# Optimization experiments

Hardware: AMD Instinct MI355X
Metric: run time of the kernel (lower is better)

## Reference

```python
import jax, jax.numpy as jnp
import numpy as np

D = 768; H = 12; L = 6; B = 8; S = 256; DH = D // H
_SCALE = 1.0 / float(np.sqrt(D))
_SCALE_FFN2 = 1.0 / float(np.sqrt(4 * D))


def _ln(x, g, b):
    m = jnp.mean(x, axis=-1, keepdims=True)
    v = jnp.mean((x - m) ** 2, axis=-1, keepdims=True)
    return (x - m) / jnp.sqrt(v + 1e-12) * g + b


def _mhsa(q_in, k_in, v_in, w, bias, mask, scale):
    # w: [3, D, D], bias: [3, D]; mask: [B, S_k]
    def proj(t, W, b):
        return (t @ W + b).reshape(t.shape[0], t.shape[1], H, DH).transpose(0, 2, 1, 3)
    q = proj(q_in, w[0], bias[0])
    k = proj(k_in, w[1], bias[1])
    v = proj(v_in, w[2], bias[2])
    s = jnp.einsum('bhqd,bhkd->bhqk', q, k) * scale
    s = s - 10000.0 * (1.0 - mask[:, None, None, :].astype(s.dtype))
    p = jax.nn.softmax(s, axis=-1)
    h = jnp.einsum('bhqk,bhkd->bhqd', p, v)
    return h.transpose(0, 2, 1, 3).reshape(q_in.shape[0], q_in.shape[1], D)


def _ffn(x, w1, b1, w2, b2):
    return jax.nn.gelu(x @ w1 + b1, approximate=False) @ w2 + b2


def setup_inputs() -> dict:
    key = jax.random.key(0)
    ks = jax.random.split(key, 16)
    inp = {
        'x': jax.random.normal(ks[0], (B, S, D), jnp.float32),
        'y': jax.random.normal(ks[1], (B, S, D), jnp.float32),
        'x_mask': jnp.ones((B, S), jnp.int32),
        'y_mask': jnp.ones((B, S), jnp.int32),
        'ax_w': jax.random.normal(ks[2], (L, 3, D, D), jnp.float32) * _SCALE,
        'ax_b': jnp.zeros((L, 3, D), jnp.float32),
        'cx_w': jax.random.normal(ks[3], (L, 3, D, D), jnp.float32) * _SCALE,
        'cx_b': jnp.zeros((L, 3, D), jnp.float32),
        'fx_w1': jax.random.normal(ks[4], (L, D, 4 * D), jnp.float32) * _SCALE,
        'fx_b1': jnp.zeros((L, 4 * D), jnp.float32),
        'fx_w2': jax.random.normal(ks[5], (L, 4 * D, D), jnp.float32) * _SCALE_FFN2,
        'fx_b2': jnp.zeros((L, D), jnp.float32),
        'ay_w': jax.random.normal(ks[6], (L, 3, D, D), jnp.float32) * _SCALE,
        'ay_b': jnp.zeros((L, 3, D), jnp.float32),
        'cy_w': jax.random.normal(ks[7], (L, 3, D, D), jnp.float32) * _SCALE,
        'cy_b': jnp.zeros((L, 3, D), jnp.float32),
        'fy_w1': jax.random.normal(ks[8], (L, D, 4 * D), jnp.float32) * _SCALE,
        'fy_b1': jnp.zeros((L, 4 * D), jnp.float32),
        'fy_w2': jax.random.normal(ks[9], (L, 4 * D, D), jnp.float32) * _SCALE_FFN2,
        'fy_b2': jnp.zeros((L, D), jnp.float32),
        'lnx_g': jnp.ones((3, D), jnp.float32),
        'lnx_b': jnp.zeros((3, D), jnp.float32),
        'lny_g': jnp.ones((3, D), jnp.float32),
        'lny_b': jnp.zeros((3, D), jnp.float32),
    }
    return inp


def reference(x, y, x_mask, y_mask, ax_w, ax_b, cx_w, cx_b, fx_w1, fx_b1, fx_w2, fx_b2,
              ay_w, ay_b, cy_w, cy_b, fy_w1, fy_b1, fy_w2, fy_b2,
              lnx_g, lnx_b, lny_g, lny_b):
    inv_sqrt_dh = 1.0 / float(np.sqrt(DH))
    params = dict(ax_w=ax_w, ax_b=ax_b, cx_w=cx_w, cx_b=cx_b,
                  fx_w1=fx_w1, fx_b1=fx_b1, fx_w2=fx_w2, fx_b2=fx_b2,
                  ay_w=ay_w, ay_b=ay_b, cy_w=cy_w, cy_b=cy_b,
                  fy_w1=fy_w1, fy_b1=fy_b1, fy_w2=fy_w2, fy_b2=fy_b2)

    def layer(carry, p):
        xc, yc = carry
        xc = _ln(xc + _mhsa(xc, xc, xc, p['ax_w'], p['ax_b'], x_mask, inv_sqrt_dh), lnx_g[0], lnx_b[0])
        yc = _ln(yc + _mhsa(yc, yc, yc, p['ay_w'], p['ay_b'], y_mask, inv_sqrt_dh), lny_g[0], lny_b[0])
        xc = _ln(xc + _mhsa(xc, yc, yc, p['cx_w'], p['cx_b'], y_mask, inv_sqrt_dh), lnx_g[1], lnx_b[1])
        yc = _ln(yc + _mhsa(yc, xc, xc, p['cy_w'], p['cy_b'], x_mask, inv_sqrt_dh), lny_g[1], lny_b[1])
        xc = _ln(xc + _ffn(xc, p['fx_w1'], p['fx_b1'], p['fx_w2'], p['fx_b2']), lnx_g[2], lnx_b[2])
        yc = _ln(yc + _ffn(yc, p['fy_w1'], p['fy_b1'], p['fy_w2'], p['fy_b2']), lny_g[2], lny_b[2])
        return (xc, yc), None

    (x, y), _ = jax.lax.scan(layer, (x, y), params)
    return jnp.stack([x, y])  # [2, B, S, D]
```

## Files before the change

kernel.cpp:

```cpp
#include <hip/hip_runtime.h>
#include <math.h>

constexpr int D = 768;
constexpr int H = 12;
constexpr int L = 6;
constexpr int B = 8;
constexpr int S = 256;
constexpr int DH = 64;
constexpr int M = B * S;
constexpr int D4 = 4 * D;

typedef _Float16 v2h __attribute__((ext_vector_type(2)));
typedef _Float16 v4h __attribute__((ext_vector_type(4)));
typedef _Float16 v8h __attribute__((ext_vector_type(8)));
typedef __fp16 f16x2 __attribute__((ext_vector_type(2)));
typedef float v4f __attribute__((ext_vector_type(4)));

__device__ inline void cvt_split(float x, float y, v2h& hi, v2h& lo) {
    f16x2 h = __builtin_amdgcn_cvt_pkrtz(x, y);
    float rx = x - (float)h[0];
    float ry = y - (float)h[1];
    f16x2 l = __builtin_amdgcn_cvt_pkrtz(rx, ry);
    hi = __builtin_bit_cast(v2h, h);
    lo = __builtin_bit_cast(v2h, l);
}

__global__ __launch_bounds__(256) void gemm_mfma(
    const float* __restrict__ Aq0, const float* __restrict__ Akv0,
    const float* __restrict__ W0,  const float* __restrict__ bias0, float* __restrict__ C0,
    const float* __restrict__ Aq1, const float* __restrict__ Akv1,
    const float* __restrict__ W1,  const float* __restrict__ bias1, float* __restrict__ C1,
    int qsplit, int Kstride, int kchunk, int N, int n_per_mat, int nblks, int act, int atomic)
{
    const int z = blockIdx.z;
    const float* __restrict__ Aq  = z ? Aq1  : Aq0;
    const float* __restrict__ Akv = z ? Akv1 : Akv0;
    const float* __restrict__ Wb  = z ? W1   : W0;
    const float* __restrict__ biasz = z ? bias1 : bias0;
    float* __restrict__ C = z ? C1 : C0;

    const int bx = blockIdx.x;
    const int nb = bx % nblks;
    const int kpart = bx / nblks;
    const int n0 = nb * 128;
    const int m0 = blockIdx.y * 128;
    const float* __restrict__ A = ((n0 < qsplit) ? Aq : Akv) + (size_t)kpart * kchunk;
    const int sub = n0 / n_per_mat;
    const int nc0 = n0 - sub * n_per_mat;
    const float* __restrict__ W = Wb + (size_t)sub * Kstride * n_per_mat
                                     + (size_t)kpart * kchunk * n_per_mat;
    const float* __restrict__ bias = (kpart == 0) ? biasz : nullptr;

    const int tid = threadIdx.x;
    const int lane = tid & 63;
    const int wave = tid >> 6;
    const int wm = (wave & 1) * 64;
    const int wn = (wave >> 1) * 64;

    __shared__ _Float16 sm[4 * 128 * 40];
    _Float16* Ah = sm;
    _Float16* Al = sm + 128 * 40;
    _Float16* Bh = sm + 2 * 128 * 40;
    _Float16* Bl = sm + 3 * 128 * 40;

    v4f acc[4][4];
    #pragma unroll
    for (int i = 0; i < 4; ++i)
        #pragma unroll
        for (int j = 0; j < 4; ++j)
            acc[i][j] = (v4f){0.f, 0.f, 0.f, 0.f};

    const int ar = tid >> 3;
    const int ac = (tid & 7) * 4;
    const int bn = tid & 127;
    const int bk0 = (tid >> 7) * 16;

    const int fm = lane & 15;
    const int fk = (lane >> 4) * 8;

    float4 av[4], av2[4];
    float bv[16], bv2[16];
    #pragma unroll
    for (int i = 0; i < 4; ++i)
        av[i] = *(const float4*)(A + (size_t)(m0 + ar + 32 * i) * Kstride + ac);
    #pragma unroll
    for (int j = 0; j < 16; ++j)
        bv[j] = W[(size_t)(bk0 + j) * n_per_mat + nc0 + bn];

    for (int k0 = 0; k0 < kchunk; k0 += 32) {
        __syncthreads();

        #pragma unroll
        for (int i = 0; i < 4; ++i) {
            v2h h0, l0, h1, l1;
            cvt_split(av[i].x, av[i].y, h0, l0);
            cvt_split(av[i].z, av[i].w, h1, l1);
            v4h hh, ll;
            hh[0] = h0[0]; hh[1] = h0[1]; hh[2] = h1[0]; hh[3] = h1[1];
            ll[0] = l0[0]; ll[1] = l0[1]; ll[2] = l1[0]; ll[3] = l1[1];
            *(v4h*)&Ah[(ar + 32 * i) * 40 + ac] = hh;
            *(v4h*)&Al[(ar + 32 * i) * 40 + ac] = ll;
        }
        {
            v8h bha, bhb, bla, blb;
            #pragma unroll
            for (int j = 0; j < 4; ++j) {
                v2h h, l;
                cvt_split(bv[2 * j], bv[2 * j + 1], h, l);
                bha[2 * j] = h[0]; bha[2 * j + 1] = h[1];
                bla[2 * j] = l[0]; bla[2 * j + 1] = l[1];
            }
            #pragma unroll
            for (int j = 0; j < 4; ++j) {
                v2h h, l;
                cvt_split(bv[8 + 2 * j], bv[8 + 2 * j + 1], h, l);
                bhb[2 * j] = h[0]; bhb[2 * j + 1] = h[1];
                blb[2 * j] = l[0]; blb[2 * j + 1] = l[1];
            }
            *(v8h*)&Bh[bn * 40 + bk0] = bha;
            *(v8h*)&Bh[bn * 40 + bk0 + 8] = bhb;
            *(v8h*)&Bl[bn * 40 + bk0] = bla;
            *(v8h*)&Bl[bn * 40 + bk0 + 8] = blb;
        }
        __syncthreads();

        if (k0 + 32 < kchunk) {
            #pragma unroll
            for (int i = 0; i < 4; ++i)
                av2[i] = *(const float4*)(A + (size_t)(m0 + ar + 32 * i) * Kstride + k0 + 32 + ac);
            #pragma unroll
            for (int j = 0; j < 16; ++j)
                bv2[j] = W[(size_t)(k0 + 32 + bk0 + j) * n_per_mat + nc0 + bn];
        }

        v8h fah[4], fal[4], fbh[4], fbl[4];
        #pragma unroll
        for (int i = 0; i < 4; ++i) {
            fah[i] = *(v8h*)&Ah[(wm + i * 16 + fm) * 40 + fk];
            fal[i] = *(v8h*)&Al[(wm + i * 16 + fm) * 40 + fk];
        }
        #pragma unroll
        for (int j = 0; j < 4; ++j) {
            fbh[j] = *(v8h*)&Bh[(wn + j * 16 + fm) * 40 + fk];
            fbl[j] = *(v8h*)&Bl[(wn + j * 16 + fm) * 40 + fk];
        }
        #pragma unroll
        for (int i = 0; i < 4; ++i)
            #pragma unroll
            for (int j = 0; j < 4; ++j) {
                acc[i][j] = __builtin_amdgcn_mfma_f32_16x16x32_f16(fah[i], fbh[j], acc[i][j], 0, 0, 0);
                acc[i][j] = __builtin_amdgcn_mfma_f32_16x16x32_f16(fah[i], fbl[j], acc[i][j], 0, 0, 0);
                acc[i][j] = __builtin_amdgcn_mfma_f32_16x16x32_f16(fal[i], fbh[j], acc[i][j], 0, 0, 0);
            }

        #pragma unroll
        for (int i = 0; i < 4; ++i) av[i] = av2[i];
        #pragma unroll
        for (int j = 0; j < 16; ++j) bv[j] = bv2[j];
    }

    const int er = (lane >> 4) * 4;
    const int ec = lane & 15;
    #pragma unroll
    for (int j = 0; j < 4; ++j) {
        const int col = n0 + wn + j * 16 + ec;
        const float bs = bias ? bias[col] : 0.0f;
        #pragma unroll
        for (int i = 0; i < 4; ++i) {
            #pragma unroll
            for (int r = 0; r < 4; ++r) {
                const int row = m0 + wm + i * 16 + er + r;
                float v = acc[i][j][r] + bs;
                if (act == 1)
                    v = 0.5f * v * (1.0f + erff(v * 0.7071067811865476f));
                if (atomic)
                    atomicAdd(&C[(size_t)row * N + col], v);
                else
                    C[(size_t)row * N + col] = v;
            }
        }
    }
}

__global__ __launch_bounds__(256) void attn_kernel(
    const float* __restrict__ qkv0, const int* __restrict__ mask0, float* __restrict__ hout0,
    const float* __restrict__ qkv1, const int* __restrict__ mask1, float* __restrict__ hout1)
{
    const float* __restrict__ qkv = blockIdx.z ? qkv1 : qkv0;
    const int* __restrict__ mask = blockIdx.z ? mask1 : mask0;
    float* __restrict__ hout = blockIdx.z ? hout1 : hout0;

    const int blk = blockIdx.x;
    const int qt = blk & 3;
    const int bh = blk >> 2;
    const int head = bh % H;
    const int b = bh / H;
    const int tid = threadIdx.x;
    const int wave = tid >> 6;
    const int lane = tid & 63;
    const int qloc = lane & 15;
    const int rg = lane >> 4;

    __shared__ _Float16 KVh[64 * 72];
    __shared__ _Float16 KVl[64 * 72];
    __shared__ _Float16 Ph[4][16 * 72];
    __shared__ _Float16 Pl[4][16 * 72];
    __shared__ float mpen[256];

    mpen[tid] = -10000.0f * (1.0f - (float)mask[b * S + tid]);

    const int qrow = b * S + qt * 64 + wave * 16 + qloc;
    const float* qptr = qkv + (size_t)qrow * 2304 + head * DH + rg * 8;
    v8h qh[2], ql[2];
    #pragma unroll
    for (int ks = 0; ks < 2; ++ks) {
        float4 a = *(const float4*)(qptr + ks * 32);
        float4 c = *(const float4*)(qptr + ks * 32 + 4);
        v2h h, l;
        v8h hh, ll;
        cvt_split(a.x, a.y, h, l); hh[0] = h[0]; hh[1] = h[1]; ll[0] = l[0]; ll[1] = l[1];
        cvt_split(a.z, a.w, h, l); hh[2] = h[0]; hh[3] = h[1]; ll[2] = l[0]; ll[3] = l[1];
        cvt_split(c.x, c.y, h, l); hh[4] = h[0]; hh[5] = h[1]; ll[4] = l[0]; ll[5] = l[1];
        cvt_split(c.z, c.w, h, l); hh[6] = h[0]; hh[7] = h[1]; ll[6] = l[0]; ll[7] = l[1];
        qh[ks] = hh; ql[ks] = ll;
    }

    v4f acc_s[16];
    #pragma unroll
    for (int i = 0; i < 16; ++i) acc_s[i] = (v4f){0.f, 0.f, 0.f, 0.f};

    const float* kbase = qkv + 768 + head * DH;
    const float* vbase = qkv + 1536 + head * DH;

    const int skey = tid & 63;
    const int sseg = (tid >> 6) * 16;
    #pragma unroll
    for (int t = 0; t < 4; ++t) {
        __syncthreads();
        {
            const float* src = kbase + (size_t)(b * S + t * 64 + skey) * 2304 + sseg;
            float4 a = ((const float4*)src)[0];
            float4 c = ((const float4*)src)[1];
            float4 e = ((const float4*)src)[2];
            float4 f = ((const float4*)src)[3];
            v2h h, l;
            v8h hA, lA, hB, lB;
            cvt_split(a.x, a.y, h, l); hA[0] = h[0]; hA[1] = h[1]; lA[0] = l[0]; lA[1] = l[1];
            cvt_split(a.z, a.w, h, l); hA[2] = h[0]; hA[3] = h[1]; lA[2] = l[0]; lA[3] = l[1];
            cvt_split(c.x, c.y, h, l); hA[4] = h[0]; hA[5] = h[1]; lA[4] = l[0]; lA[5] = l[1];
            cvt_split(c.z, c.w, h, l); hA[6] = h[0]; hA[7] = h[1]; lA[6] = l[0]; lA[7] = l[1];
            cvt_split(e.x, e.y, h, l); hB[0] = h[0]; hB[1] = h[1]; lB[0] = l[0]; lB[1] = l[1];
            cvt_split(e.z, e.w, h, l); hB[2] = h[0]; hB[3] = h[1]; lB[2] = l[0]; lB[3] = l[1];
            cvt_split(f.x, f.y, h, l); hB[4] = h[0]; hB[5] = h[1]; lB[4] = l[0]; lB[5] = l[1];
            cvt_split(f.z, f.w, h, l); hB[6] = h[0]; hB[7] = h[1]; lB[6] = l[0]; lB[7] = l[1];
            *(v8h*)&KVh[skey * 72 + sseg] = hA;
            *(v8h*)&KVh[skey * 72 + sseg + 8] = hB;
            *(v8h*)&KVl[skey * 72 + sseg] = lA;
            *(v8h*)&KVl[skey * 72 + sseg + 8] = lB;
        }
        __syncthreads();
        #pragma unroll
        for (int sub = 0; sub < 4; ++sub) {
            v8h kh[2], kl[2];
            #pragma unroll
            for (int ks = 0; ks < 2; ++ks) {
                kh[ks] = *(v8h*)&KVh[(sub * 16 + qloc) * 72 + ks * 32 + rg * 8];
                kl[ks] = *(v8h*)&KVl[(sub * 16 + qloc) * 72 + ks * 32 + rg * 8];
            }
            v4f acc = acc_s[t * 4 + sub];
            #pragma unroll
            for (int ks = 0; ks < 2; ++ks) {
                acc = __builtin_amdgcn_mfma_f32_16x16x32_f16(kh[ks], qh[ks], acc, 0, 0, 0);
                acc = __builtin_amdgcn_mfma_f32_16x16x32_f16(kh[ks], ql[ks], acc, 0, 0, 0);
                acc = __builtin_amdgcn_mfma_f32_16x16x32_f16(kl[ks], qh[ks], acc, 0, 0, 0);
            }
            acc_s[t * 4 + sub] = acc;
        }
    }

    float mx = -3.0e38f;
    #pragma unroll
    for (int mt = 0; mt < 16; ++mt) {
        float4 mp = *(const float4*)&mpen[mt * 16 + rg * 4];
        v4f s = acc_s[mt];
        s[0] = s[0] * 0.125f + mp.x;
        s[1] = s[1] * 0.125f + mp.y;
        s[2] = s[2] * 0.125f + mp.z;
        s[3] = s[3] * 0.125f + mp.w;
        acc_s[mt] = s;
        mx = fmaxf(mx, fmaxf(fmaxf(s[0], s[1]), fmaxf(s[2], s[3])));
    }
    mx = fmaxf(mx, __shfl_xor(mx, 16, 64));
    mx = fmaxf(mx, __shfl_xor(mx, 32, 64));
    float sum = 0.f;
    #pragma unroll
    for (int mt = 0; mt < 16; ++mt) {
        v4f s = acc_s[mt];
        s[0] = __expf(s[0] - mx);
        s[1] = __expf(s[1] - mx);
        s[2] = __expf(s[2] - mx);
        s[3] = __expf(s[3] - mx);
        acc_s[mt] = s;
        sum += (s[0] + s[1]) + (s[2] + s[3]);
    }
    sum += __shfl_xor(sum, 16, 64);
    sum += __shfl_xor(sum, 32, 64);
    const float inv = 1.0f / sum;

    v4f acc_o[4];
    #pragma unroll
    for (int j = 0; j < 4; ++j) acc_o[j] = (v4f){0.f, 0.f, 0.f, 0.f};

    const int vk4 = (tid & 15) * 4;
    const int vd4 = (tid >> 4) * 4;
    #pragma unroll
    for (int t = 0; t < 4; ++t) {
        __syncthreads();
        #pragma unroll
        for (int sub = 0; sub < 4; ++sub) {
            v4f p = acc_s[t * 4 + sub];
            v2h h01, l01, h23, l23;
            cvt_split(p[0], p[1], h01, l01);
            cvt_split(p[2], p[3], h23, l23);
            *(v2h*)&Ph[wave][qloc * 72 + sub * 16 + rg * 4] = h01;
            *(v2h*)&Ph[wave][qloc * 72 + sub * 16 + rg * 4 + 2] = h23;
            *(v2h*)&Pl[wave][qloc * 72 + sub * 16 + rg * 4] = l01;
            *(v2h*)&Pl[wave][qloc * 72 + sub * 16 + rg * 4 + 2] = l23;
        }
        {
            v4h rh[4], rl[4];
            #pragma unroll
            for (int i = 0; i < 4; ++i) {
                const float4 vv = *(const float4*)(vbase + (size_t)(b * S + t * 64 + vk4 + i) * 2304 + vd4);
                v2h h0, l0, h1, l1;
                cvt_split(vv.x, vv.y, h0, l0);
                cvt_split(vv.z, vv.w, h1, l1);
                rh[0][i] = h0[0]; rh[1][i] = h0[1]; rh[2][i] = h1[0]; rh[3][i] = h1[1];
                rl[0][i] = l0[0]; rl[1][i] = l0[1]; rl[2][i] = l1[0]; rl[3][i] = l1[1];
            }
            #pragma unroll
            for (int j = 0; j < 4; ++j) {
                *(v4h*)&KVh[(vd4 + j) * 72 + vk4] = rh[j];
                *(v4h*)&KVl[(vd4 + j) * 72 + vk4] = rl[j];
            }
        }
        __syncthreads();
        v8h pah[2], pal[2];
        #pragma unroll
        for (int ks = 0; ks < 2; ++ks) {
            pah[ks] = *(v8h*)&Ph[wave][qloc * 72 + ks * 32 + rg * 8];
            pal[ks] = *(v8h*)&Pl[wave][qloc * 72 + ks * 32 + rg * 8];
        }
        #pragma unroll
        for (int j = 0; j < 4; ++j) {
            v4f acc = acc_o[j];
            #pragma unroll
            for (int ks = 0; ks < 2; ++ks) {
                v8h vbh = *(v8h*)&KVh[(j * 16 + qloc) * 72 + ks * 32 + rg * 8];
                v8h vbl = *(v8h*)&KVl[(j * 16 + qloc) * 72 + ks * 32 + rg * 8];
                acc = __builtin_amdgcn_mfma_f32_16x16x32_f16(pah[ks], vbh, acc, 0, 0, 0);
                acc = __builtin_amdgcn_mfma_f32_16x16x32_f16(pah[ks], vbl, acc, 0, 0, 0);
                acc = __builtin_amdgcn_mfma_f32_16x16x32_f16(pal[ks], vbh, acc, 0, 0, 0);
            }
            acc_o[j] = acc;
        }
    }

    #pragma unroll
    for (int r = 0; r < 4; ++r) {
        const float invr = __shfl(inv, rg * 4 + r, 64);
        const size_t row = (size_t)(b * S + qt * 64 + wave * 16 + rg * 4 + r);
        #pragma unroll
        for (int j = 0; j < 4; ++j)
            hout[row * D + head * DH + j * 16 + qloc] = acc_o[j][r] * invr;
    }
}

__global__ __launch_bounds__(256) void ln_res_kernel(
    float* __restrict__ x0, const float* __restrict__ h0,
    const float* __restrict__ g0, const float* __restrict__ bb0,
    float* __restrict__ x1, const float* __restrict__ h1,
    const float* __restrict__ g1, const float* __restrict__ bb1)
{
    float* __restrict__ x = blockIdx.y ? x1 : x0;
    const float* __restrict__ h = blockIdx.y ? h1 : h0;
    const float* __restrict__ g = blockIdx.y ? g1 : g0;
    const float* __restrict__ bb = blockIdx.y ? bb1 : bb0;

    const int row = blockIdx.x;
    const int tid = threadIdx.x;
    const int wave = tid >> 6;
    const int lane = tid & 63;
    __shared__ float red[4];

    float v[3];
    #pragma unroll
    for (int i = 0; i < 3; ++i) {
        int c = tid + 256 * i;
        v[i] = x[(size_t)row * D + c] + h[(size_t)row * D + c];
    }
    float s = v[0] + v[1] + v[2];
    #pragma unroll
    for (int o = 32; o > 0; o >>= 1) s += __shfl_xor(s, o, 64);
    if (lane == 0) red[wave] = s;
    __syncthreads();
    const float mean = (red[0] + red[1] + red[2] + red[3]) * (1.0f / 768.0f);

    float qs = 0.f;
    #pragma unroll
    for (int i = 0; i < 3; ++i) { float d = v[i] - mean; qs += d * d; }
    #pragma unroll
    for (int o = 32; o > 0; o >>= 1) qs += __shfl_xor(qs, o, 64);
    __syncthreads();
    if (lane == 0) red[wave] = qs;
    __syncthreads();
    const float var = (red[0] + red[1] + red[2] + red[3]) * (1.0f / 768.0f);
    const float rstd = rsqrtf(var + 1e-12f);

    #pragma unroll
    for (int i = 0; i < 3; ++i) {
        int c = tid + 256 * i;
        x[(size_t)row * D + c] = (v[i] - mean) * rstd * g[c] + bb[c];
    }
}

extern "C" void kernel_launch(void* const* d_in, const int* in_sizes, int n_in,
                              void* d_out, int out_size, void* d_ws, size_t ws_size,
                              hipStream_t stream)
{
    const float* x    = (const float*)d_in[0];
    const float* y    = (const float*)d_in[1];
    const int*   xm   = (const int*)d_in[2];
    const int*   ym   = (const int*)d_in[3];
    const float* ax_w = (const float*)d_in[4];
    const float* ax_b = (const float*)d_in[5];
    const float* cx_w = (const float*)d_in[6];
    const float* cx_b = (const float*)d_in[7];
    const float* fx_w1 = (const float*)d_in[8];
    const float* fx_b1 = (const float*)d_in[9];
    const float* fx_w2 = (const float*)d_in[10];
    const float* fx_b2 = (const float*)d_in[11];
    const float* ay_w = (const float*)d_in[12];
    const float* ay_b = (const float*)d_in[13];
    const float* cy_w = (const float*)d_in[14];
    const float* cy_b = (const float*)d_in[15];
    const float* fy_w1 = (const float*)d_in[16];
    const float* fy_b1 = (const float*)d_in[17];
    const float* fy_w2 = (const float*)d_in[18];
    const float* fy_b2 = (const float*)d_in[19];
    const float* lnx_g = (const float*)d_in[20];
    const float* lnx_b = (const float*)d_in[21];
    const float* lny_g = (const float*)d_in[22];
    const float* lny_b = (const float*)d_in[23];

    float* xc = (float*)d_out;
    float* yc = xc + (size_t)M * D;

    const size_t need = ((size_t)2 * M * D4 + (size_t)2 * M * D) * sizeof(float);
    const bool big = ws_size >= need;
    float* ws0 = (float*)d_ws;
    float* qkvx = ws0;
    float* qkvy = big ? ws0 + (size_t)M * D4 : ws0;
    float* hbx = ws0 + (big ? (size_t)2 * M * D4 : (size_t)M * D4);
    float* hby = big ? hbx + (size_t)M * D : hbx;

    (void)hipMemcpyAsync(xc, x, (size_t)M * D * sizeof(float), hipMemcpyDeviceToDevice, stream);
    (void)hipMemcpyAsync(yc, y, (size_t)M * D * sizeof(float), hipMemcpyDeviceToDevice, stream);

    const dim3 blk(256);
    constexpr int KSPLIT = 4;

    auto qkv_gemm = [&](const float* aq0, const float* akv0, const float* w0, const float* bi0, float* c0,
                        const float* aq1, const float* akv1, const float* w1, const float* bi1, float* c1,
                        int nz) {
        gemm_mfma<<<dim3(2304 / 128, M / 128, nz), blk, 0, stream>>>(
            aq0, akv0, w0, bi0, c0, aq1, akv1, w1, bi1, c1,
            768, D, D, 2304, 768, 2304 / 128, 0, 0);
    };
    auto ffn1_gemm = [&](const float* a0, const float* w0, const float* bi0, float* c0,
                         const float* a1, const float* w1, const float* bi1, float* c1, int nz) {
        gemm_mfma<<<dim3(D4 / 128, M / 128, nz), blk, 0, stream>>>(
            a0, a0, w0, bi0, c0, a1, a1, w1, bi1, c1,
            0, D, D, D4, D4, D4 / 128, 1, 0);
    };
    auto ffn2_gemm_split = [&](const float* a0, const float* w0, const float* bi0, float* c0,
                               const float* a1, const float* w1, const float* bi1, float* c1, int nz) {
        gemm_mfma<<<dim3((D / 128) * KSPLIT, M / 128, nz), blk, 0, stream>>>(
            a0, a0, w0, bi0, c0, a1, a1, w1, bi1, c1,
            0, D4, D4 / KSPLIT, D, D, D / 128, 0, 1);
    };
    auto ffn2_gemm_seq = [&](const float* a0, const float* w0, const float* bi0, float* c0,
                             const float* a1, const float* w1, const float* bi1, float* c1, int nz) {
        gemm_mfma<<<dim3(D / 128, M / 128, nz), blk, 0, stream>>>(
            a0, a0, w0, bi0, c0, a1, a1, w1, bi1, c1,
            0, D4, D4, D, D, D / 128, 0, 0);
    };
    auto attn = [&](const float* q0, const int* m0_, float* h0,
                    const float* q1, const int* m1_, float* h1, int nz) {
        attn_kernel<<<dim3(B * H * 4, 1, nz), blk, 0, stream>>>(q0, m0_, h0, q1, m1_, h1);
    };
    auto ln = [&](float* x0, const float* h0, const float* g0, const float* b0,
                  float* x1, const float* h1, const float* g1, const float* b1, int ny) {
        ln_res_kernel<<<dim3(M, ny), blk, 0, stream>>>(x0, h0, g0, b0, x1, h1, g1, b1);
    };

    for (int l = 0; l < L; ++l) {
        const size_t wo = (size_t)l * 3 * D * D;
        const size_t bo = (size_t)l * 3 * D;
        const size_t f1o = (size_t)l * D * D4;
        const size_t f1bo = (size_t)l * D4;
        const size_t f2o = (size_t)l * D4 * D;
        const size_t f2bo = (size_t)l * D;

        if (big) {
            qkv_gemm(xc, xc, ax_w + wo, ax_b + bo, qkvx,
                     yc, yc, ay_w + wo, ay_b + bo, qkvy, 2);
            attn(qkvx, xm, hbx, qkvy, ym, hby, 2);
            ln(xc, hbx, lnx_g, lnx_b, yc, hby, lny_g, lny_b, 2);
            qkv_gemm(xc, yc, cx_w + wo, cx_b + bo, qkvx,
                     xc, yc, cx_w + wo, cx_b + bo, qkvx, 1);
            attn(qkvx, ym, hbx, qkvx, ym, hbx, 1);
            ln(xc, hbx, lnx_g + D, lnx_b + D, xc, hbx, lnx_g + D, lnx_b + D, 1);
            qkv_gemm(yc, xc, cy_w + wo, cy_b + bo, qkvy,
                     yc, xc, cy_w + wo, cy_b + bo, qkvy, 1);
            attn(qkvy, xm, hby, qkvy, xm, hby, 1);
            ln(yc, hby, lny_g + D, lny_b + D, yc, hby, lny_g + D, lny_b + D, 1);
            ffn1_gemm(xc, fx_w1 + f1o, fx_b1 + f1bo, qkvx,
                      yc, fy_w1 + f1o, fy_b1 + f1bo, qkvy, 2);
            (void)hipMemsetAsync(hbx, 0, (size_t)2 * M * D * sizeof(float), stream);
            ffn2_gemm_split(qkvx, fx_w2 + f2o, fx_b2 + f2bo, hbx,
                            qkvy, fy_w2 + f2o, fy_b2 + f2bo, hby, 2);
            ln(xc, hbx, lnx_g + 2 * D, lnx_b + 2 * D,
               yc, hby, lny_g + 2 * D, lny_b + 2 * D, 2);
        } else {
            qkv_gemm(xc, xc, ax_w + wo, ax_b + bo, qkvx, xc, xc, ax_w + wo, ax_b + bo, qkvx, 1);
            attn(qkvx, xm, hbx, qkvx, xm, hbx, 1);
            ln(xc, hbx, lnx_g, lnx_b, xc, hbx, lnx_g, lnx_b, 1);
            qkv_gemm(yc, yc, ay_w + wo, ay_b + bo, qkvy, yc, yc, ay_w + wo, ay_b + bo, qkvy, 1);
            attn(qkvy, ym, hby, qkvy, ym, hby, 1);
            ln(yc, hby, lny_g, lny_b, yc, hby, lny_g, lny_b, 1);
            qkv_gemm(xc, yc, cx_w + wo, cx_b + bo, qkvx, xc, yc, cx_w + wo, cx_b + bo, qkvx, 1);
            attn(qkvx, ym, hbx, qkvx, ym, hbx, 1);
            ln(xc, hbx, lnx_g + D, lnx_b + D, xc, hbx, lnx_g + D, lnx_b + D, 1);
            qkv_gemm(yc, xc, cy_w + wo, cy_b + bo, qkvy, yc, xc, cy_w + wo, cy_b + bo, qkvy, 1);
            attn(qkvy, xm, hby, qkvy, xm, hby, 1);
            ln(yc, hby, lny_g + D, lny_b + D, yc, hby, lny_g + D, lny_b + D, 1);
            ffn1_gemm(xc, fx_w1 + f1o, fx_b1 + f1bo, qkvx, xc, fx_w1 + f1o, fx_b1 + f1bo, qkvx, 1);
            ffn2_gemm_seq(qkvx, fx_w2 + f2o, fx_b2 + f2bo, hbx, qkvx, fx_w2 + f2o, fx_b2 + f2bo, hbx, 1);
            ln(xc, hbx, lnx_g + 2 * D, lnx_b + 2 * D, xc, hbx, lnx_g + 2 * D, lnx_b + 2 * D, 1);
            ffn1_gemm(yc, fy_w1 + f1o, fy_b1 + f1bo, qkvy, yc, fy_w1 + f1o, fy_b1 + f1bo, qkvy, 1);
            ffn2_gemm_seq(qkvy, fy_w2 + f2o, fy_b2 + f2bo, hby, qkvy, fy_w2 + f2o, fy_b2 + f2bo, hby, 1);
            ln(yc, hby, lny_g + 2 * D, lny_b + 2 * D, yc, hby, lny_g + 2 * D, lny_b + 2 * D, 1);
        }
    }
}
```

Baseline: 3.026 ms.

## Store activations as pre-split fp16 hi/lo pairs produced by producer epilogues

```diff
diff --git a/kernel.cpp b/kernel.cpp
--- a/kernel.cpp
+++ b/kernel.cpp
@@ -25,26 +25,39 @@
     lo = __builtin_bit_cast(v2h, l);
 }
 
+__device__ inline void split1(float v, _Float16& hi, _Float16& lo) {
+    f16x2 h = __builtin_amdgcn_cvt_pkrtz(v, v);
+    float r = v - (float)h[0];
+    f16x2 l = __builtin_amdgcn_cvt_pkrtz(r, r);
+    hi = (_Float16)h[0];
+    lo = (_Float16)l[0];
+}
+
 __global__ __launch_bounds__(256) void gemm_mfma(
-    const float* __restrict__ Aq0, const float* __restrict__ Akv0,
-    const float* __restrict__ W0,  const float* __restrict__ bias0, float* __restrict__ C0,
-    const float* __restrict__ Aq1, const float* __restrict__ Akv1,
-    const float* __restrict__ W1,  const float* __restrict__ bias1, float* __restrict__ C1,
-    int qsplit, int Kstride, int kchunk, int N, int n_per_mat, int nblks, int act, int atomic)
+    const _Float16* __restrict__ Aq0, const _Float16* __restrict__ Akv0,
+    const float* __restrict__ W0,  const float* __restrict__ bias0,
+    float* __restrict__ C0, _Float16* __restrict__ P0,
+    const _Float16* __restrict__ Aq1, const _Float16* __restrict__ Akv1,
+    const float* __restrict__ W1,  const float* __restrict__ bias1,
+    float* __restrict__ C1, _Float16* __restrict__ P1,
+    int qsplit, int Kstride, int kchunk, int N, int n_per_mat, int nblks,
+    int act, int atomic, int outp, long asize, long csize)
 {
     const int z = blockIdx.z;
-    const float* __restrict__ Aq  = z ? Aq1  : Aq0;
-    const float* __restrict__ Akv = z ? Akv1 : Akv0;
+    const _Float16* __restrict__ Aq  = z ? Aq1  : Aq0;
+    const _Float16* __restrict__ Akv = z ? Akv1 : Akv0;
     const float* __restrict__ Wb  = z ? W1   : W0;
     const float* __restrict__ biasz = z ? bias1 : bias0;
     float* __restrict__ C = z ? C1 : C0;
+    _Float16* __restrict__ Ph_g = z ? P1 : P0;
 
     const int bx = blockIdx.x;
     const int nb = bx % nblks;
     const int kpart = bx / nblks;
     const int n0 = nb * 128;
     const int m0 = blockIdx.y * 128;
-    const float* __restrict__ A = ((n0 < qsplit) ? Aq : Akv) + (size_t)kpart * kchunk;
+    const _Float16* __restrict__ Ah_g = ((n0 < qsplit) ? Aq : Akv) + (size_t)kpart * kchunk;
+    const _Float16* __restrict__ Al_g = Ah_g + asize;
     const int sub = n0 / n_per_mat;
     const int nc0 = n0 - sub * n_per_mat;
     const float* __restrict__ W = Wb + (size_t)sub * Kstride * n_per_mat
@@ -70,19 +83,21 @@
         for (int j = 0; j < 4; ++j)
             acc[i][j] = (v4f){0.f, 0.f, 0.f, 0.f};
 
-    const int ar = tid >> 3;
-    const int ac = (tid & 7) * 4;
+    const int ar = tid >> 2;
+    const int ac = (tid & 3) * 8;
     const int bn = tid & 127;
     const int bk0 = (tid >> 7) * 16;
 
     const int fm = lane & 15;
     const int fk = (lane >> 4) * 8;
 
-    float4 av[4], av2[4];
+    v8h avh[2], avl[2], avh2[2], avl2[2];
     float bv[16], bv2[16];
     #pragma unroll
-    for (int i = 0; i < 4; ++i)
-        av[i] = *(const float4*)(A + (size_t)(m0 + ar + 32 * i) * Kstride + ac);
+    for (int i = 0; i < 2; ++i) {
+        avh[i] = *(const v8h*)(Ah_g + (size_t)(m0 + ar + 64 * i) * Kstride + ac);
+        avl[i] = *(const v8h*)(Al_g + (size_t)(m0 + ar + 64 * i) * Kstride + ac);
+    }
     #pragma unroll
     for (int j = 0; j < 16; ++j)
         bv[j] = W[(size_t)(bk0 + j) * n_per_mat + nc0 + bn];
@@ -91,15 +106,9 @@
         __syncthreads();
 
         #pragma unroll
-        for (int i = 0; i < 4; ++i) {
-            v2h h0, l0, h1, l1;
-            cvt_split(av[i].x, av[i].y, h0, l0);
-            cvt_split(av[i].z, av[i].w, h1, l1);
-            v4h hh, ll;
-            hh[0] = h0[0]; hh[1] = h0[1]; hh[2] = h1[0]; hh[3] = h1[1];
-            ll[0] = l0[0]; ll[1] = l0[1]; ll[2] = l1[0]; ll[3] = l1[1];
-            *(v4h*)&Ah[(ar + 32 * i) * 40 + ac] = hh;
-            *(v4h*)&Al[(ar + 32 * i) * 40 + ac] = ll;
+        for (int i = 0; i < 2; ++i) {
+            *(v8h*)&Ah[(ar + 64 * i) * 40 + ac] = avh[i];
+            *(v8h*)&Al[(ar + 64 * i) * 40 + ac] = avl[i];
         }
         {
             v8h bha, bhb, bla, blb;
@@ -126,8 +135,10 @@
 
         if (k0 + 32 < kchunk) {
             #pragma unroll
-            for (int i = 0; i < 4; ++i)
-                av2[i] = *(const float4*)(A + (size_t)(m0 + ar + 32 * i) * Kstride + k0 + 32 + ac);
+            for (int i = 0; i < 2; ++i) {
+                avh2[i] = *(const v8h*)(Ah_g + (size_t)(m0 + ar + 64 * i) * Kstride + k0 + 32 + ac);
+                avl2[i] = *(const v8h*)(Al_g + (size_t)(m0 + ar + 64 * i) * Kstride + k0 + 32 + ac);
+            }
             #pragma unroll
             for (int j = 0; j < 16; ++j)
                 bv2[j] = W[(size_t)(k0 + 32 + bk0 + j) * n_per_mat + nc0 + bn];
@@ -154,7 +165,7 @@
             }
 
         #pragma unroll
-        for (int i = 0; i < 4; ++i) av[i] = av2[i];
+        for (int i = 0; i < 2; ++i) { avh[i] = avh2[i]; avl[i] = avl2[i]; }
         #pragma unroll
         for (int j = 0; j < 16; ++j) bv[j] = bv2[j];
     }
@@ -173,22 +184,29 @@
                 float v = acc[i][j][r] + bs;
                 if (act == 1)
                     v = 0.5f * v * (1.0f + erff(v * 0.7071067811865476f));
-                if (atomic)
+                if (outp) {
+                    _Float16 hi, lo;
+                    split1(v, hi, lo);
+                    Ph_g[(size_t)row * N + col] = hi;
+                    Ph_g[(size_t)row * N + col + csize] = lo;
+                } else if (atomic) {
                     atomicAdd(&C[(size_t)row * N + col], v);
-                else
+                } else {
                     C[(size_t)row * N + col] = v;
+                }
             }
         }
     }
 }
 
 __global__ __launch_bounds__(256) void attn_kernel(
-    const float* __restrict__ qkv0, const int* __restrict__ mask0, float* __restrict__ hout0,
-    const float* __restrict__ qkv1, const int* __restrict__ mask1, float* __restrict__ hout1)
+    const _Float16* __restrict__ qkvh0, const int* __restrict__ mask0, float* __restrict__ hout0,
+    const _Float16* __restrict__ qkvh1, const int* __restrict__ mask1, float* __restrict__ hout1)
 {
-    const float* __restrict__ qkv = blockIdx.z ? qkv1 : qkv0;
+    const _Float16* __restrict__ qkvh = blockIdx.z ? qkvh1 : qkvh0;
     const int* __restrict__ mask = blockIdx.z ? mask1 : mask0;
     float* __restrict__ hout = blockIdx.z ? hout1 : hout0;
+    const _Float16* __restrict__ qkvl = qkvh + (size_t)M * 2304;
 
     const int blk = blockIdx.x;
     const int qt = blk & 3;
@@ -210,27 +228,17 @@
     mpen[tid] = -10000.0f * (1.0f - (float)mask[b * S + tid]);
 
     const int qrow = b * S + qt * 64 + wave * 16 + qloc;
-    const float* qptr = qkv + (size_t)qrow * 2304 + head * DH + rg * 8;
+    const size_t qoff = (size_t)qrow * 2304 + head * DH + rg * 8;
     v8h qh[2], ql[2];
     #pragma unroll
     for (int ks = 0; ks < 2; ++ks) {
-        float4 a = *(const float4*)(qptr + ks * 32);
-        float4 c = *(const float4*)(qptr + ks * 32 + 4);
-        v2h h, l;
-        v8h hh, ll;
-        cvt_split(a.x, a.y, h, l); hh[0] = h[0]; hh[1] = h[1]; ll[0] = l[0]; ll[1] = l[1];
-        cvt_split(a.z, a.w, h, l); hh[2] = h[0]; hh[3] = h[1]; ll[2] = l[0]; ll[3] = l[1];
-        cvt_split(c.x, c.y, h, l); hh[4] = h[0]; hh[5] = h[1]; ll[4] = l[0]; ll[5] = l[1];
-        cvt_split(c.z, c.w, h, l); hh[6] = h[0]; hh[7] = h[1]; ll[6] = l[0]; ll[7] = l[1];
-        qh[ks] = hh; ql[ks] = ll;
+        qh[ks] = *(const v8h*)(qkvh + qoff + ks * 32);
+        ql[ks] = *(const v8h*)(qkvl + qoff + ks * 32);
     }
 
     v4f acc_s[16];
     #pragma unroll
     for (int i = 0; i < 16; ++i) acc_s[i] = (v4f){0.f, 0.f, 0.f, 0.f};
-
-    const float* kbase = qkv + 768 + head * DH;
-    const float* vbase = qkv + 1536 + head * DH;
 
     const int skey = tid & 63;
     const int sseg = (tid >> 6) * 16;
@@ -238,21 +246,11 @@
     for (int t = 0; t < 4; ++t) {
         __syncthreads();
         {
-            const float* src = kbase + (size_t)(b * S + t * 64 + skey) * 2304 + sseg;
-            float4 a = ((const float4*)src)[0];
-            float4 c = ((const float4*)src)[1];
-            float4 e = ((const float4*)src)[2];
-            float4 f = ((const float4*)src)[3];
-            v2h h, l;
-            v8h hA, lA, hB, lB;
-            cvt_split(a.x, a.y, h, l); hA[0] = h[0]; hA[1] = h[1]; lA[0] = l[0]; lA[1] = l[1];
-            cvt_split(a.z, a.w, h, l); hA[2] = h[0]; hA[3] = h[1]; lA[2] = l[0]; lA[3] = l[1];
-            cvt_split(c.x, c.y, h, l); hA[4] = h[0]; hA[5] = h[1]; lA[4] = l[0]; lA[5] = l[1];
-            cvt_split(c.z, c.w, h, l); hA[6] = h[0]; hA[7] = h[1]; lA[6] = l[0]; lA[7] = l[1];
-            cvt_split(e.x, e.y, h, l); hB[0] = h[0]; hB[1] = h[1]; lB[0] = l[0]; lB[1] = l[1];
-            cvt_split(e.z, e.w, h, l); hB[2] = h[0]; hB[3] = h[1]; lB[2] = l[0]; lB[3] = l[1];
-            cvt_split(f.x, f.y, h, l); hB[4] = h[0]; hB[5] = h[1]; lB[4] = l[0]; lB[5] = l[1];
-            cvt_split(f.z, f.w, h, l); hB[6] = h[0]; hB[7] = h[1]; lB[6] = l[0]; lB[7] = l[1];
+            const size_t off = (size_t)(b * S + t * 64 + skey) * 2304 + 768 + head * DH + sseg;
+            const v8h hA = ((const v8h*)(qkvh + off))[0];
+            const v8h hB = ((const v8h*)(qkvh + off))[1];
+            const v8h lA = ((const v8h*)(qkvl + off))[0];
+            const v8h lB = ((const v8h*)(qkvl + off))[1];
             *(v8h*)&KVh[skey * 72 + sseg] = hA;
             *(v8h*)&KVh[skey * 72 + sseg + 8] = hB;
             *(v8h*)&KVl[skey * 72 + sseg] = lA;
@@ -331,12 +329,11 @@
             v4h rh[4], rl[4];
             #pragma unroll
             for (int i = 0; i < 4; ++i) {
-                const float4 vv = *(const float4*)(vbase + (size_t)(b * S + t * 64 + vk4 + i) * 2304 + vd4);
-                v2h h0, l0, h1, l1;
-                cvt_split(vv.x, vv.y, h0, l0);
-                cvt_split(vv.z, vv.w, h1, l1);
-                rh[0][i] = h0[0]; rh[1][i] = h0[1]; rh[2][i] = h1[0]; rh[3][i] = h1[1];
-                rl[0][i] = l0[0]; rl[1][i] = l0[1]; rl[2][i] = l1[0]; rl[3][i] = l1[1];
+                const size_t off = (size_t)(b * S + t * 64 + vk4 + i) * 2304 + 1536 + head * DH + vd4;
+                const v4h hv = *(const v4h*)(qkvh + off);
+                const v4h lv = *(const v4h*)(qkvl + off);
+                rh[0][i] = hv[0]; rh[1][i] = hv[1]; rh[2][i] = hv[2]; rh[3][i] = hv[3];
+                rl[0][i] = lv[0]; rl[1][i] = lv[1]; rl[2][i] = lv[2]; rl[3][i] = lv[3];
             }
             #pragma unroll
             for (int j = 0; j < 4; ++j) {
@@ -378,14 +375,16 @@
 
 __global__ __launch_bounds__(256) void ln_res_kernel(
     float* __restrict__ x0, const float* __restrict__ h0,
-    const float* __restrict__ g0, const float* __restrict__ bb0,
+    const float* __restrict__ g0, const float* __restrict__ bb0, _Float16* __restrict__ p0,
     float* __restrict__ x1, const float* __restrict__ h1,
-    const float* __restrict__ g1, const float* __restrict__ bb1)
+    const float* __restrict__ g1, const float* __restrict__ bb1, _Float16* __restrict__ p1)
 {
     float* __restrict__ x = blockIdx.y ? x1 : x0;
     const float* __restrict__ h = blockIdx.y ? h1 : h0;
     const float* __restrict__ g = blockIdx.y ? g1 : g0;
     const float* __restrict__ bb = blockIdx.y ? bb1 : bb0;
+    _Float16* __restrict__ ph = blockIdx.y ? p1 : p0;
+    _Float16* __restrict__ pl = ph + (size_t)M * D;
 
     const int row = blockIdx.x;
     const int tid = threadIdx.x;
@@ -420,8 +419,32 @@
     #pragma unroll
     for (int i = 0; i < 3; ++i) {
         int c = tid + 256 * i;
-        x[(size_t)row * D + c] = (v[i] - mean) * rstd * g[c] + bb[c];
-    }
+        float o = (v[i] - mean) * rstd * g[c] + bb[c];
+        x[(size_t)row * D + c] = o;
+        _Float16 hi, lo;
+        split1(o, hi, lo);
+        ph[(size_t)row * D + c] = hi;
+        pl[(size_t)row * D + c] = lo;
+    }
+}
+
+__global__ __launch_bounds__(256) void split_kernel(
+    const float* __restrict__ in0, _Float16* __restrict__ p0,
+    const float* __restrict__ in1, _Float16* __restrict__ p1, long n)
+{
+    const float* __restrict__ in = blockIdx.y ? in1 : in0;
+    _Float16* __restrict__ ph = blockIdx.y ? p1 : p0;
+    _Float16* __restrict__ pl = ph + n;
+    const size_t idx = ((size_t)blockIdx.x * 256 + threadIdx.x) * 4;
+    float4 v = *(const float4*)(in + idx);
+    v2h h0, l0, h1, l1;
+    cvt_split(v.x, v.y, h0, l0);
+    cvt_split(v.z, v.w, h1, l1);
+    v4h hh, ll;
+    hh[0] = h0[0]; hh[1] = h0[1]; hh[2] = h1[0]; hh[3] = h1[1];
+    ll[0] = l0[0]; ll[1] = l0[1]; ll[2] = l1[0]; ll[3] = l1[1];
+    *(v4h*)(ph + idx) = hh;
+    *(v4h*)(pl + idx) = ll;
 }
 
 extern "C" void kernel_launch(void* const* d_in, const int* in_sizes, int n_in,
@@ -456,52 +479,61 @@
     float* xc = (float*)d_out;
     float* yc = xc + (size_t)M * D;
 
-    const size_t need = ((size_t)2 * M * D4 + (size_t)2 * M * D) * sizeof(float);
+    const size_t need = ((size_t)2 * M * D4 + (size_t)4 * M * D) * sizeof(float);
     const bool big = ws_size >= need;
     float* ws0 = (float*)d_ws;
     float* qkvx = ws0;
     float* qkvy = big ? ws0 + (size_t)M * D4 : ws0;
-    float* hbx = ws0 + (big ? (size_t)2 * M * D4 : (size_t)M * D4);
+    float* hbx = big ? qkvy + (size_t)M * D4 : qkvx + (size_t)M * D4;
     float* hby = big ? hbx + (size_t)M * D : hbx;
+    _Float16* xp = (_Float16*)(hby + (size_t)M * D);
+    _Float16* yp = xp + (size_t)2 * M * D;
+
+    _Float16* qpx = (_Float16*)qkvx;
+    _Float16* qpy = (_Float16*)qkvy;
 
     (void)hipMemcpyAsync(xc, x, (size_t)M * D * sizeof(float), hipMemcpyDeviceToDevice, stream);
     (void)hipMemcpyAsync(yc, y, (size_t)M * D * sizeof(float), hipMemcpyDeviceToDevice, stream);
+    split_kernel<<<dim3(M * D / 1024, 2), dim3(256), 0, stream>>>(x, xp, y, yp, (long)M * D);
 
     const dim3 blk(256);
     constexpr int KSPLIT = 4;
 
-    auto qkv_gemm = [&](const float* aq0, const float* akv0, const float* w0, const float* bi0, float* c0,
-                        const float* aq1, const float* akv1, const float* w1, const float* bi1, float* c1,
+    const long aD  = (long)M * D;
+    const long aD4 = (long)M * D4;
+
+    auto qkv_gemm = [&](const _Float16* aq0, const _Float16* akv0, const float* w0, const float* bi0, _Float16* p0,
+                        const _Float16* aq1, const _Float16* akv1, const float* w1, const float* bi1, _Float16* p1,
                         int nz) {
         gemm_mfma<<<dim3(2304 / 128, M / 128, nz), blk, 0, stream>>>(
-            aq0, akv0, w0, bi0, c0, aq1, akv1, w1, bi1, c1,
-            768, D, D, 2304, 768, 2304 / 128, 0, 0);
+            aq0, akv0, w0, bi0, nullptr, p0, aq1, akv1, w1, bi1, nullptr, p1,
+            768, D, D, 2304, 768, 2304 / 128, 0, 0, 1, aD, (long)M * 2304);
     };
-    auto ffn1_gemm = [&](const float* a0, const float* w0, const float* bi0, float* c0,
-                         const float* a1, const float* w1, const float* bi1, float* c1, int nz) {
+    auto ffn1_gemm = [&](const _Float16* a0, const float* w0, const float* bi0, _Float16* p0,
+                         const _Float16* a1, const float* w1, const float* bi1, _Float16* p1, int nz) {
         gemm_mfma<<<dim3(D4 / 128, M / 128, nz), blk, 0, stream>>>(
-            a0, a0, w0, bi0, c0, a1, a1, w1, bi1, c1,
-            0, D, D, D4, D4, D4 / 128, 1, 0);
+            a0, a0, w0, bi0, nullptr, p0, a1, a1, w1, bi1, nullptr, p1,
+            0, D, D, D4, D4, D4 / 128, 1, 0, 1, aD, aD4);
     };
-    auto ffn2_gemm_split = [&](const float* a0, const float* w0, const float* bi0, float* c0,
-                               const float* a1, const float* w1, const float* bi1, float* c1, int nz) {
+    auto ffn2_gemm_split = [&](const _Float16* a0, const float* w0, const float* bi0, float* c0,
+                               const _Float16* a1, const float* w1, const float* bi1, float* c1, int nz) {
         gemm_mfma<<<dim3((D / 128) * KSPLIT, M / 128, nz), blk, 0, stream>>>(
-            a0, a0, w0, bi0, c0, a1, a1, w1, bi1, c1,
-            0, D4, D4 / KSPLIT, D, D, D / 128, 0, 1);
+            a0, a0, w0, bi0, c0, nullptr, a1, a1, w1, bi1, c1, nullptr,
+            0, D4, D4 / KSPLIT, D, D, D / 128, 0, 1, 0, aD4, 0);
     };
-    auto ffn2_gemm_seq = [&](const float* a0, const float* w0, const float* bi0, float* c0,
-                             const float* a1, const float* w1, const float* bi1, float* c1, int nz) {
+    auto ffn2_gemm_seq = [&](const _Float16* a0, const float* w0, const float* bi0, float* c0,
+                             const _Float16* a1, const float* w1, const float* bi1, float* c1, int nz) {
         gemm_mfma<<<dim3(D / 128, M / 128, nz), blk, 0, stream>>>(
-            a0, a0, w0, bi0, c0, a1, a1, w1, bi1, c1,
-            0, D4, D4, D, D, D / 128, 0, 0);
+            a0, a0, w0, bi0, c0, nullptr, a1, a1, w1, bi1, c1, nullptr,
+            0, D4, D4, D, D, D / 128, 0, 0, 0, aD4, 0);
     };
-    auto attn = [&](const float* q0, const int* m0_, float* h0,
-                    const float* q1, const int* m1_, float* h1, int nz) {
+    auto attn = [&](const _Float16* q0, const int* m0_, float* h0,
+                    const _Float16* q1, const int* m1_, float* h1, int nz) {
         attn_kernel<<<dim3(B * H * 4, 1, nz), blk, 0, stream>>>(q0, m0_, h0, q1, m1_, h1);
     };
-    auto ln = [&](float* x0, const float* h0, const float* g0, const float* b0,
-                  float* x1, const float* h1, const float* g1, const float* b1, int ny) {
-        ln_res_kernel<<<dim3(M, ny), blk, 0, stream>>>(x0, h0, g0, b0, x1, h1, g1, b1);
+    auto ln = [&](float* x0, const float* h0, const float* g0, const float* b0, _Float16* p0,
+                  float* x1, const float* h1, const float* g1, const float* b1, _Float16* p1, int ny) {
+        ln_res_kernel<<<dim3(M, ny), blk, 0, stream>>>(x0, h0, g0, b0, p0, x1, h1, g1, b1, p1);
     };
 
     for (int l = 0; l < L; ++l) {
@@ -513,44 +545,44 @@
         const size_t f2bo = (size_t)l * D;
 
         if (big) {
-            qkv_gemm(xc, xc, ax_w + wo, ax_b + bo, qkvx,
-                     yc, yc, ay_w + wo, ay_b + bo, qkvy, 2);
-            attn(qkvx, xm, hbx, qkvy, ym, hby, 2);
-            ln(xc, hbx, lnx_g, lnx_b, yc, hby, lny_g, lny_b, 2);
-            qkv_gemm(xc, yc, cx_w + wo, cx_b + bo, qkvx,
-                     xc, yc, cx_w + wo, cx_b + bo, qkvx, 1);
-            attn(qkvx, ym, hbx, qkvx, ym, hbx, 1);
-            ln(xc, hbx, lnx_g + D, lnx_b + D, xc, hbx, lnx_g + D, lnx_b + D, 1);
-            qkv_gemm(yc, xc, cy_w + wo, cy_b + bo, qkvy,
-                     yc, xc, cy_w + wo, cy_b + bo, qkvy, 1);
-            attn(qkvy, xm, hby, qkvy, xm, hby, 1);
-            ln(yc, hby, lny_g + D, lny_b + D, yc, hby, lny_g + D, lny_b + D, 1);
-            ffn1_gemm(xc, fx_w1 + f1o, fx_b1 + f1bo, qkvx,
-                      yc, fy_w1 + f1o, fy_b1 + f1bo, qkvy, 2);
+            qkv_gemm(xp, xp, ax_w + wo, ax_b + bo, qpx,
+                     yp, yp, ay_w + wo, ay_b + bo, qpy, 2);
+            attn(qpx, xm, hbx, qpy, ym, hby, 2);
+            ln(xc, hbx, lnx_g, lnx_b, xp, yc, hby, lny_g, lny_b, yp, 2);
+            qkv_gemm(xp, yp, cx_w + wo, cx_b + bo, qpx,
+                     xp, yp, cx_w + wo, cx_b + bo, qpx, 1);
+            attn(qpx, ym, hbx, qpx, ym, hbx, 1);
+            ln(xc, hbx, lnx_g + D, lnx_b + D, xp, xc, hbx, lnx_g + D, lnx_b + D, xp, 1);
+            qkv_gemm(yp, xp, cy_w + wo, cy_b + bo, qpy,
+                     yp, xp, cy_w + wo, cy_b + bo, qpy, 1);
+            attn(qpy, xm, hby, qpy, xm, hby, 1);
+            ln(yc, hby, lny_g + D, lny_b + D, yp, yc, hby, lny_g + D, lny_b + D, yp, 1);
+            ffn1_gemm(xp, fx_w1 + f1o, fx_b1 + f1bo, qpx,
+                      yp, fy_w1 + f1o, fy_b1 + f1bo, qpy, 2);
             (void)hipMemsetAsync(hbx, 0, (size_t)2 * M * D * sizeof(float), stream);
-            ffn2_gemm_split(qkvx, fx_w2 + f2o, fx_b2 + f2bo, hbx,
-                            qkvy, fy_w2 + f2o, fy_b2 + f2bo, hby, 2);
-            ln(xc, hbx, lnx_g + 2 * D, lnx_b + 2 * D,
-               yc, hby, lny_g + 2 * D, lny_b + 2 * D, 2);
+            ffn2_gemm_split(qpx, fx_w2 + f2o, fx_b2 + f2bo, hbx,
+                            qpy, fy_w2 + f2o, fy_b2 + f2bo, hby, 2);
+            ln(xc, hbx, lnx_g + 2 * D, lnx_b + 2 * D, xp,
+               yc, hby, lny_g + 2 * D, lny_b + 2 * D, yp, 2);
         } else {
-            qkv_gemm(xc, xc, ax_w + wo, ax_b + bo, qkvx, xc, xc, ax_w + wo, ax_b + bo, qkvx, 1);
-            attn(qkvx, xm, hbx, qkvx, xm, hbx, 1);
-            ln(xc, hbx, lnx_g, lnx_b, xc, hbx, lnx_g, lnx_b, 1);
-            qkv_gemm(yc, yc, ay_w + wo, ay_b + bo, qkvy, yc, yc, ay_w + wo, ay_b + bo, qkvy, 1);
-            attn(qkvy, ym, hby, qkvy, ym, hby, 1);
-            ln(yc, hby, lny_g, lny_b, yc, hby, lny_g, lny_b, 1);
-            qkv_gemm(xc, yc, cx_w + wo, cx_b + bo, qkvx, xc, yc, cx_w + wo, cx_b + bo, qkvx, 1);
-            attn(qkvx, ym, hbx, qkvx, ym, hbx, 1);
-            ln(xc, hbx, lnx_g + D, lnx_b + D, xc, hbx, lnx_g + D, lnx_b + D, 1);
-            qkv_gemm(yc, xc, cy_w + wo, cy_b + bo, qkvy, yc, xc, cy_w + wo, cy_b + bo, qkvy, 1);
-            attn(qkvy, xm, hby, qkvy, xm, hby, 1);
-            ln(yc, hby, lny_g + D, lny_b + D, yc, hby, lny_g + D, lny_b + D, 1);
-            ffn1_gemm(xc, fx_w1 + f1o, fx_b1 + f1bo, qkvx, xc, fx_w1 + f1o, fx_b1 + f1bo, qkvx, 1);
-            ffn2_gemm_seq(qkvx, fx_w2 + f2o, fx_b2 + f2bo, hbx, qkvx, fx_w2 + f2o, fx_b2 + f2bo, hbx, 1);
-            ln(xc, hbx, lnx_g + 2 * D, lnx_b + 2 * D, xc, hbx, lnx_g + 2 * D, lnx_b + 2 * D, 1);
-            ffn1_gemm(yc, fy_w1 + f1o, fy_b1 + f1bo, qkvy, yc, fy_w1 + f1o, fy_b1 + f1bo, qkvy, 1);
-            ffn2_gemm_seq(qkvy, fy_w2 + f2o, fy_b2 + f2bo, hby, qkvy, fy_w2 + f2o, fy_b2 + f2bo, hby, 1);
-            ln(yc, hby, lny_g + 2 * D, lny_b + 2 * D, yc, hby, lny_g + 2 * D, lny_b + 2 * D, 1);
-        }
-    }
-}
+            qkv_gemm(xp, xp, ax_w + wo, ax_b + bo, qpx, xp, xp, ax_w + wo, ax_b + bo, qpx, 1);
+            attn(qpx, xm, hbx, qpx, xm, hbx, 1);
+            ln(xc, hbx, lnx_g, lnx_b, xp, xc, hbx, lnx_g, lnx_b, xp, 1);
+            qkv_gemm(yp, yp, ay_w + wo, ay_b + bo, qpy, yp, yp, ay_w + wo, ay_b + bo, qpy, 1);
+            attn(qpy, ym, hby, qpy, ym, hby, 1);
+            ln(yc, hby, lny_g, lny_b, yp, yc, hby, lny_g, lny_b, yp, 1);
+            qkv_gemm(xp, yp, cx_w + wo, cx_b + bo, qpx, xp, yp, cx_w + wo, cx_b + bo, qpx, 1);
+            attn(qpx, ym, hbx, qpx, ym, hbx, 1);
+            ln(xc, hbx, lnx_g + D, lnx_b + D, xp, xc, hbx, lnx_g + D, lnx_b + D, xp, 1);
+            qkv_gemm(yp, xp, cy_w + wo, cy_b + bo, qpy, yp, xp, cy_w + wo, cy_b + bo, qpy, 1);
+            attn(qpy, xm, hby, qpy, xm, hby, 1);
+            ln(yc, hby, lny_g + D, lny_b + D, yp, yc, hby, lny_g + D, lny_b + D, yp, 1);
+            ffn1_gemm(xp, fx_w1 + f1o, fx_b1 + f1bo, qpx, xp, fx_w1 + f1o, fx_b1 + f1bo, qpx, 1);
+            ffn2_gemm_seq(qpx, fx_w2 + f2o, fx_b2 + f2bo, hbx, qpx, fx_w2 + f2o, fx_b2 + f2bo, hbx, 1);
+            ln(xc, hbx, lnx_g + 2 * D, lnx_b + 2 * D, xp, xc, hbx, lnx_g + 2 * D, lnx_b + 2 * D, xp, 1);
+            ffn1_gemm(yp, fy_w1 + f1o, fy_b1 + f1bo, qpy, yp, fy_w1 + f1o, fy_b1 + f1bo, qpy, 1);
+            ffn2_gemm_seq(qpy, fy_w2 + f2o, fy_b2 + f2bo, hby, qpy, fy_w2 + f2o, fy_b2 + f2bo, hby, 1);
+            ln(yc, hby, lny_g + 2 * D, lny_b + 2 * D, yp, yc, hby, lny_g + 2 * D, lny_b + 2 * D, yp, 1);
+        }
+    }
+}
```

Measured after the change: 3.246 ms. +7.3%, slower.
